# Performance work log

Measured on AMD Instinct MI355X. Metric: run time of the kernel, lower is better.

The kernel has to match this reference:

```python
import jax, jax.numpy as jnp
import numpy as np

EPS_ATTN = 1e-8  # self.eps is undefined in the torch source; standard slot-attention value
LN_EPS = 1e-5


def _ln(x, g=None, b=None, axes=(-1,)):
    m = x.mean(axes, keepdims=True)
    v = ((x - m) ** 2).mean(axes, keepdims=True)
    y = (x - m) * jax.lax.rsqrt(v + LN_EPS)
    return y * g + b if g is not None else y


def setup_inputs() -> dict:
    key = jax.random.key(0)
    ks = jax.random.split(key, 16)
    B, N, S, d, dh = 16, 4096, 8, 64, 128

    def w(k, shape, fan_in):
        return jax.random.normal(k, shape, jnp.float32) / np.float32(np.sqrt(fan_in))

    return {
        "inputs": jax.random.normal(ks[0], (B, N, d + 2), jnp.float32),
        "slots": jax.random.normal(ks[1], (S, d + 4), jnp.float32),
        "Wq": w(ks[2], (d, d), d),
        "Wk": w(ks[3], (d, d), d),
        "Wv": w(ks[4], (d, d), d),
        "Wg": w(ks[5], (d, 2), 2),
        "bg": jnp.zeros((d,), jnp.float32),
        "ln_pos_g": jnp.ones((d,), jnp.float32),
        "ln_pos_b": jnp.zeros((d,), jnp.float32),
        "W1": w(ks[6], (dh, d), d),
        "b1": jnp.zeros((dh,), jnp.float32),
        "W2": w(ks[7], (d, dh), dh),
        "b2": jnp.zeros((d,), jnp.float32),
        "W_ih": w(ks[8], (3 * d, d), d),
        "W_hh": w(ks[9], (3 * d, d), d),
        "b_ih": jnp.zeros((3 * d,), jnp.float32),
        "b_hh": jnp.zeros((3 * d,), jnp.float32),
        "ln_mlp_g": jnp.ones((d,), jnp.float32),
        "ln_mlp_b": jnp.zeros((d,), jnp.float32),
        "W3": w(ks[10], (dh, d), d),
        "b3": jnp.zeros((dh,), jnp.float32),
        "W4": w(ks[11], (d, dh), dh),
        "b4": jnp.zeros((d,), jnp.float32),
        "ln_slot_g": jnp.ones((d,), jnp.float32),
        "ln_slot_b": jnp.zeros((d,), jnp.float32),
        "n_iters": 3,
    }


def reference(inputs, slots, Wq, Wk, Wv, Wg, bg, ln_pos_g, ln_pos_b, W1, b1, W2, b2,
              W_ih, W_hh, b_ih, b_hh, ln_mlp_g, ln_mlp_b, W3, b3, W4, b4,
              ln_slot_g, ln_slot_b, n_iters):
    feats, grids = inputs[..., :-2], inputs[..., -2:]          # (B,N,d), (B,N,2)
    sl, pos, sc = slots[..., :-4], slots[..., -4:-2], slots[..., -2:]
    B, N, _ = feats.shape
    S, d = sl.shape
    scale = d ** (-0.5)

    slots = jnp.broadcast_to(sl, (B, S, d))
    positions = jnp.clip(jnp.broadcast_to(pos, (B, S, 2)), -1.0, 1.0)
    scales = jnp.clip(jnp.broadcast_to(sc, (B, S, 2)), 1e-3, 2.0)

    k = feats @ Wk.T                                           # (B,N,d)
    v = feats @ Wv.T

    def pos_mlp(x):  # LayerNorm -> Linear -> ReLU -> Linear
        h = _ln(x, ln_pos_g, ln_pos_b)
        h = jax.nn.relu(h @ W1.T + b1)
        return h @ W2.T + b2

    for i_iter in range(n_iters + 1):
        rel = (grids[:, :, None] - positions[:, None]) / scales[:, None]  # (B,N,S,2)
        rgp = rel @ Wg.T + bg                                             # (B,N,S,d)
        k_pos = pos_mlp(k[:, :, None] + rgp)                              # (B,N,S,d)
        v_pos = pos_mlp(v[:, :, None] + rgp)

        slots_n = _ln(slots, ln_slot_g, ln_slot_b)
        q = _ln(slots_n, axes=(-2, -1)) @ Wq.T                            # (B,S,d)

        dots = jnp.einsum('bsd,bnsd->bns', q, k_pos) * scale              # (B,N,S)
        attn = jax.nn.softmax(dots, axis=1) + EPS_ATTN
        attn = attn / attn.sum(axis=-1, keepdims=True)

        updates = jnp.einsum('bns,bnsd->bsd', attn, v_pos)                # (B,S,d)
        positions = jnp.einsum('bns,bnp->bsp', attn, grids)               # (B,S,2)
        spread = (grids[:, :, None] - positions[:, None]) ** 2            # (B,N,S,2)
        scales = jnp.clip(jnp.sqrt(jnp.einsum('bns,bnsp->bsp', attn, spread)), 1e-3, 2.0)

        if i_iter < n_iters:
            x = updates.reshape(-1, d)
            h = slots.reshape(-1, d)
            gi = x @ W_ih.T + b_ih
            gh = h @ W_hh.T + b_hh
            i_r, i_z, i_n = jnp.split(gi, 3, axis=-1)
            h_r, h_z, h_n = jnp.split(gh, 3, axis=-1)
            r = jax.nn.sigmoid(i_r + h_r)
            z = jax.nn.sigmoid(i_z + h_z)
            n_g = jnp.tanh(i_n + r * h_n)
            slots = ((1.0 - z) * n_g + z * h).reshape(B, S, d)
            # slot_mlp (no residual in the source)
            hmlp = jax.nn.relu(_ln(slots, ln_mlp_g, ln_mlp_b) @ W3.T + b3)
            slots = hmlp @ W4.T + b4

    return jnp.concatenate([slots, positions, scales], axis=-1)           # (B,S,d+4)
```

## Files before the change

### kernel.cpp

```cpp
#include <hip/hip_runtime.h>
#include <math.h>

#define BB 16
#define NN 4096
#define SS 8
#define DD 64
#define DHH 128
#define CIN 66
#define NITERS 3
#define LN_EPS_F 1e-5f
#define EPS_ATTN_F 1e-8f
#define QSCALE 0.125f
#define LO_SCALE 2048.0f
#define LO_INV 4.8828125e-4f

typedef __attribute__((ext_vector_type(8))) _Float16 half8;
typedef __attribute__((ext_vector_type(4))) float f32x4;
union H8 { half8 v; _Float16 u[8]; };

__device__ __forceinline__ float dot4(float4 a, float4 b) {
    return fmaf(a.x, b.x, fmaf(a.y, b.y, fmaf(a.z, b.z, a.w * b.w)));
}

__device__ __forceinline__ void split_fp16(float z, _Float16& h, _Float16& l) {
    _Float16 hh = (_Float16)z;
    float rem = (z - (float)hh) * LO_SCALE;
    h = hh;
    l = (_Float16)rem;
}

__global__ __launch_bounds__(256) void k_init_slots(
    const float* __restrict__ slots_in, float* __restrict__ slots,
    float* __restrict__ positions, float* __restrict__ scales) {
    int tid = blockIdx.x * 256 + threadIdx.x;
    if (tid < BB * SS * DD) {
        int s = (tid / DD) % SS;
        int c = tid % DD;
        slots[tid] = slots_in[s * 68 + c];
    }
    if (tid < BB * SS * 2) {
        int s = (tid >> 1) & 7;
        int p = tid & 1;
        float po = slots_in[s * 68 + 64 + p];
        positions[tid] = fminf(fmaxf(po, -1.f), 1.f);
        float sc = slots_in[s * 68 + 66 + p];
        scales[tid] = fminf(fmaxf(sc, 1e-3f), 2.f);
    }
}

__global__ __launch_bounds__(256) void k_prep_w(
    const float* __restrict__ W1, const float* __restrict__ lpg,
    const float* __restrict__ lpb, const float* __restrict__ b1,
    const float* __restrict__ Wg,
    float* __restrict__ W1p, float* __restrict__ avec, float* __restrict__ bvec,
    float* __restrict__ s1vec, float* __restrict__ b1p, float* __restrict__ wgc) {
    __shared__ float w1s[128 * 68];
    int tid = threadIdx.x;
    for (int q = 0; q < 8; q++) {
        int flat = q * 1024 + tid * 4;
        int o = flat >> 6, c = flat & 63;
        *(float4*)(w1s + o * 68 + c) = *(const float4*)(W1 + flat);
    }
    __syncthreads();
    if (tid < 128) {
        int o = tid;
        float a = 0.f, bv = 0.f, s1 = 0.f, b1a = b1[o];
        for (int c = 0; c < 64; c++) {
            float w0 = w1s[o * 68 + c];
            float w = w0 * lpg[c];
            W1p[o * 64 + c] = w;
            a = fmaf(w, Wg[2 * c], a);
            bv = fmaf(w, Wg[2 * c + 1], bv);
            s1 += w;
            b1a = fmaf(w0, lpb[c], b1a);
        }
        avec[o] = a; bvec[o] = bv; s1vec[o] = s1; b1p[o] = b1a;
    }
    if (tid == 128) {
        float mwA = 0.f, mwB = 0.f, AA = 0.f, BBv = 0.f, AB = 0.f;
        for (int c = 0; c < 64; c++) {
            float wa = Wg[2 * c], wb = Wg[2 * c + 1];
            mwA += wa; mwB += wb;
            AA = fmaf(wa, wa, AA); BBv = fmaf(wb, wb, BBv); AB = fmaf(wa, wb, AB);
        }
        wgc[0] = mwA * (1.f / 64.f);
        wgc[1] = mwB * (1.f / 64.f);
        wgc[2] = AA * (1.f / 64.f);
        wgc[3] = BBv * (1.f / 64.f);
        wgc[4] = AB * (2.f / 64.f);
    }
}

__global__ __launch_bounds__(256) void k_prep_w2(
    const float* __restrict__ W1p, const float* __restrict__ Wk,
    const float* __restrict__ Wv, const float* __restrict__ bg,
    float* __restrict__ Wall, float* __restrict__ cu) {
    int flat = blockIdx.x * 256 + threadIdx.x;
    int mat = flat >> 13, rem = flat & 8191;
    int o = rem >> 6, c = rem & 63;
    const float* Wm = mat ? Wv : Wk;
    float acc = 0.f;
    for (int d = 0; d < 64; d++)
        acc = fmaf(W1p[o * 64 + d], Wm[d * 64 + c], acc);
    Wall[flat] = acc;
    if (flat < 128) {
        float a = 0.f;
        for (int d = 0; d < 64; d++) a = fmaf(W1p[flat * 64 + d], bg[d], a);
        cu[flat] = a;
    }
}

__global__ __launch_bounds__(256) void k_prep_frag(
    const float* __restrict__ Wall, const float* __restrict__ Wk,
    const float* __restrict__ Wv,
    _Float16* __restrict__ cwh, _Float16* __restrict__ cwl,
    _Float16* __restrict__ mwh, _Float16* __restrict__ mwl) {
    int idx = blockIdx.x * 256 + threadIdx.x;
    if (idx < 2048) {
        int f = idx >> 6, lane = idx & 63;
        int m = f >> 4, rest = f & 15;
        int ot = rest >> 1, ks = rest & 1;
        int o = ot * 16 + (lane & 15);
        int k0 = ks * 32 + (lane >> 4) * 8;
        const float* src = Wall + m * 8192 + o * 64 + k0;
        #pragma unroll
        for (int j = 0; j < 8; j++) {
            _Float16 h, l;
            split_fp16(src[j], h, l);
            cwh[(size_t)f * 512 + lane * 8 + j] = h;
            cwl[(size_t)f * 512 + lane * 8 + j] = l;
        }
    } else if (idx < 3072) {
        int id2 = idx - 2048;
        int f = id2 >> 6, lane = id2 & 63;
        int m = f >> 3, rest = f & 7;
        int ot = rest >> 1, ks = rest & 1;
        int o = ot * 16 + (lane & 15);
        int k0 = ks * 32 + (lane >> 4) * 8;
        const float* src = (m ? Wv : Wk) + o * 64 + k0;
        #pragma unroll
        for (int j = 0; j < 8; j++) {
            _Float16 h, l;
            split_fp16(src[j], h, l);
            mwh[(size_t)f * 512 + lane * 8 + j] = h;
            mwl[(size_t)f * 512 + lane * 8 + j] = l;
        }
    }
}

__global__ __launch_bounds__(256) void k_prep_mfma(
    const float* __restrict__ inp,
    const _Float16* __restrict__ cwh, const _Float16* __restrict__ cwl,
    const _Float16* __restrict__ mwh, const _Float16* __restrict__ mwl,
    const float* __restrict__ cu, const float* __restrict__ bg,
    const float* __restrict__ Wg,
    float* __restrict__ uk, float* __restrict__ uv,
    float* __restrict__ kaux, float* __restrict__ vaux, float* __restrict__ gbuf) {
    int tid = threadIdx.x;
    int wv = tid >> 6, lane = tid & 63;
    int quad = lane >> 4, col = lane & 15;
    int mat = blockIdx.y;
    int rowTile = blockIdx.x * 64 + wv * 16;
    half8 ah[2], al[2];
    {
        int rA = rowTile + col;
        const float* rp = inp + (size_t)rA * CIN + quad * 8;
        #pragma unroll
        for (int ks = 0; ks < 2; ks++) {
            H8 h, l;
            #pragma unroll
            for (int q = 0; q < 4; q++) {
                float2 v = *(const float2*)(rp + ks * 32 + 2 * q);
                split_fp16(v.x, h.u[2 * q], l.u[2 * q]);
                split_fp16(v.y, h.u[2 * q + 1], l.u[2 * q + 1]);
            }
            ah[ks] = h.v; al[ks] = l.v;
        }
    }
    const _Float16* cwhm = cwh + (size_t)mat * 16 * 512;
    const _Float16* cwlm = cwl + (size_t)mat * 16 * 512;
    float* dst = mat ? uv : uk;
    float* outb = dst + (size_t)(rowTile + quad * 4) * 128 + col;
    #pragma unroll
    for (int ot = 0; ot < 8; ot++) {
        f32x4 acc1 = {0.f, 0.f, 0.f, 0.f}, acc2 = {0.f, 0.f, 0.f, 0.f};
        #pragma unroll
        for (int ks = 0; ks < 2; ks++) {
            half8 bh = *(const half8*)(cwhm + (size_t)(ot * 2 + ks) * 512 + lane * 8);
            half8 bl = *(const half8*)(cwlm + (size_t)(ot * 2 + ks) * 512 + lane * 8);
            acc1 = __builtin_amdgcn_mfma_f32_16x16x32_f16(ah[ks], bh, acc1, 0, 0, 0);
            acc2 = __builtin_amdgcn_mfma_f32_16x16x32_f16(al[ks], bh, acc2, 0, 0, 0);
            acc2 = __builtin_amdgcn_mfma_f32_16x16x32_f16(ah[ks], bl, acc2, 0, 0, 0);
        }
        float cuv = cu[ot * 16 + col];
        #pragma unroll
        for (int r = 0; r < 4; r++)
            outb[(size_t)r * 128 + ot * 16] = fmaf(acc2[r], LO_INV, acc1[r]) + cuv;
    }
    const _Float16* mwhm = mwh + (size_t)mat * 8 * 512;
    const _Float16* mwlm = mwl + (size_t)mat * 8 * 512;
    float mk[4] = {0.f, 0.f, 0.f, 0.f}, kk2[4] = {0.f, 0.f, 0.f, 0.f};
    float kA[4] = {0.f, 0.f, 0.f, 0.f}, kB[4] = {0.f, 0.f, 0.f, 0.f};
    #pragma unroll
    for (int ot = 0; ot < 4; ot++) {
        f32x4 acc1 = {0.f, 0.f, 0.f, 0.f}, acc2 = {0.f, 0.f, 0.f, 0.f};
        #pragma unroll
        for (int ks = 0; ks < 2; ks++) {
            half8 bh = *(const half8*)(mwhm + (size_t)(ot * 2 + ks) * 512 + lane * 8);
            half8 bl = *(const half8*)(mwlm + (size_t)(ot * 2 + ks) * 512 + lane * 8);
            acc1 = __builtin_amdgcn_mfma_f32_16x16x32_f16(ah[ks], bh, acc1, 0, 0, 0);
            acc2 = __builtin_amdgcn_mfma_f32_16x16x32_f16(al[ks], bh, acc2, 0, 0, 0);
            acc2 = __builtin_amdgcn_mfma_f32_16x16x32_f16(ah[ks], bl, acc2, 0, 0, 0);
        }
        int o = ot * 16 + col;
        float bgo = bg[o], wa = Wg[2 * o], wb = Wg[2 * o + 1];
        #pragma unroll
        for (int r = 0; r < 4; r++) {
            float x = fmaf(acc2[r], LO_INV, acc1[r]) + bgo;
            mk[r] += x; kk2[r] = fmaf(x, x, kk2[r]);
            kA[r] = fmaf(x, wa, kA[r]); kB[r] = fmaf(x, wb, kB[r]);
        }
    }
    #pragma unroll
    for (int off = 1; off <= 8; off <<= 1) {
        #pragma unroll
        for (int r = 0; r < 4; r++) {
            mk[r] += __shfl_xor(mk[r], off, 64);
            kk2[r] += __shfl_xor(kk2[r], off, 64);
            kA[r] += __shfl_xor(kA[r], off, 64);
            kB[r] += __shfl_xor(kB[r], off, 64);
        }
    }
    float* aux = mat ? vaux : kaux;
    if (col == 0) {
        #pragma unroll
        for (int r = 0; r < 4; r++) {
            int row = rowTile + quad * 4 + r;
            float2 g = *(const float2*)(inp + (size_t)row * CIN + 64);
            float4 m1 = {mk[r] * (1.f / 64.f), kk2[r] * (1.f / 64.f),
                         kA[r] * (1.f / 32.f), kB[r] * (1.f / 32.f)};
            float4 m2 = {g.x, g.y, 0.f, 0.f};
            *(float4*)(aux + (size_t)row * 8) = m1;
            *(float4*)(aux + (size_t)row * 8 + 4) = m2;
            if (mat == 0) {
                float2 gw = {g.x, g.y};
                *(float2*)(gbuf + (size_t)row * 2) = gw;
            }
        }
    }
}

__global__ __launch_bounds__(512) void k_slot_prep(
    const float* __restrict__ slots, const float* __restrict__ lsg,
    const float* __restrict__ lsb, const float* __restrict__ Wq,
    const float* __restrict__ W2, const float* __restrict__ b2,
    float* __restrict__ w2q, float* __restrict__ qb2) {
    __shared__ float sn[512];
    __shared__ float qv[SS][64];
    __shared__ float wsum[8], wsum2[8];
    int b = blockIdx.x, t = threadIdx.x;
    int s = t >> 6, c = t & 63;
    float x = slots[(b * SS + s) * DD + c];
    float sum = x;
    for (int off = 32; off; off >>= 1) sum += __shfl_xor(sum, off, 64);
    float m = sum * (1.f / 64.f);
    float dv = x - m;
    float vs = dv * dv;
    for (int off = 32; off; off >>= 1) vs += __shfl_xor(vs, off, 64);
    float y = dv * rsqrtf(vs * (1.f / 64.f) + LN_EPS_F) * lsg[c] + lsb[c];
    float s1 = y, s2 = y * y;
    for (int off = 32; off; off >>= 1) { s1 += __shfl_xor(s1, off, 64); s2 += __shfl_xor(s2, off, 64); }
    if (c == 0) { wsum[s] = s1; wsum2[s] = s2; }
    __syncthreads();
    float ts1 = 0.f, ts2 = 0.f;
    #pragma unroll
    for (int i = 0; i < 8; i++) { ts1 += wsum[i]; ts2 += wsum2[i]; }
    float gm = ts1 * (1.f / 512.f);
    float gv = ts2 * (1.f / 512.f) - gm * gm;
    sn[t] = (y - gm) * rsqrtf(gv + LN_EPS_F);
    __syncthreads();
    float acc = 0.f;
    for (int j4 = 0; j4 < 64; j4 += 4)
        acc += dot4(*(const float4*)&sn[s * 64 + j4], *(const float4*)(Wq + c * 64 + j4));
    qv[s][c] = acc;
    __syncthreads();
    float a0 = 0.f, a1 = 0.f;
    for (int cc = 0; cc < 64; cc++) {
        float qc = qv[s][cc];
        a0 = fmaf(qc, W2[cc * DHH + c], a0);
        a1 = fmaf(qc, W2[cc * DHH + c + 64], a1);
    }
    w2q[(b * SS + s) * DHH + c] = a0 * QSCALE;
    w2q[(b * SS + s) * DHH + c + 64] = a1 * QSCALE;
    float qb = qv[s][c] * b2[c];
    for (int off = 32; off; off >>= 1) qb += __shfl_xor(qb, off, 64);
    if (c == 0) qb2[b * SS + s] = qb * QSCALE;
}

__global__ __launch_bounds__(256) void k_pass1(
    const float* __restrict__ uk, const float* __restrict__ kaux,
    const float* __restrict__ positions, const float* __restrict__ scales,
    const float* __restrict__ avec, const float* __restrict__ bvec,
    const float* __restrict__ s1vec, const float* __restrict__ b1p,
    const float* __restrict__ wgc, const float* __restrict__ w2q,
    const float* __restrict__ qb2, float* __restrict__ dots) {
    int tid = threadIdx.x;
    int chunk = blockIdx.x, b = blockIdx.y;
    int wv = tid >> 6, lane = tid & 63, rh = lane >> 5, ol = lane & 31;
    int o4 = ol * 4;
    float4 a4 = *(const float4*)(avec + o4);
    float4 bv4 = *(const float4*)(bvec + o4);
    float4 s14 = *(const float4*)(s1vec + o4);
    float4 b14 = *(const float4*)(b1p + o4);
    float mwA = wgc[0], mwB = wgc[1], AA = wgc[2], BBc = wgc[3], AB2 = wgc[4];
    float p0[8], p1[8], rc0[8], rc1[8], qb[8];
    float4 wq[8];
    #pragma unroll
    for (int s = 0; s < 8; s++) {
        int bs = b * 8 + s;
        p0[s] = positions[bs * 2]; p1[s] = positions[bs * 2 + 1];
        rc0[s] = 1.f / scales[bs * 2]; rc1[s] = 1.f / scales[bs * 2 + 1];
        qb[s] = qb2[bs];
        wq[s] = *(const float4*)(w2q + (size_t)bs * DHH + o4);
    }
    int row0 = chunk * 64 + wv * 16 + rh;
    size_t rg = (size_t)b * NN + row0;
    float4 m1 = *(const float4*)(kaux + rg * 8);
    float4 m2 = *(const float4*)(kaux + rg * 8 + 4);
    float4 u4 = *(const float4*)(uk + rg * 128 + o4);
    for (int st = 0; st < 8; st++) {
        float4 n1, n2, nu;
        if (st < 7) {
            size_t rgn = rg + (size_t)(st + 1) * 2;
            n1 = *(const float4*)(kaux + rgn * 8);
            n2 = *(const float4*)(kaux + rgn * 8 + 4);
            nu = *(const float4*)(uk + rgn * 128 + o4);
        }
        int row = row0 + st * 2;
        #pragma unroll
        for (int s = 0; s < 8; s++) {
            float rel0 = (m2.x - p0[s]) * rc0[s];
            float rel1 = (m2.y - p1[s]) * rc1[s];
            float m = fmaf(rel1, mwB, fmaf(rel0, mwA, m1.x));
            float q2 = fmaf(rel0, fmaf(rel0, AA, m1.z), m1.y);
            q2 = fmaf(rel1, fmaf(rel1, BBc, m1.w), q2);
            q2 = fmaf(rel0 * rel1, AB2, q2);
            float var = fmaf(-m, m, q2);
            float rstd = rsqrtf(fmaxf(var, 0.f) + LN_EPS_F);
            float p = 0.f, t, h;
            t = fmaf(-m, s14.x, u4.x); t = fmaf(rel0, a4.x, t); t = fmaf(rel1, bv4.x, t);
            h = fmaf(rstd, t, b14.x); p = fmaf(fmaxf(h, 0.f), wq[s].x, p);
            t = fmaf(-m, s14.y, u4.y); t = fmaf(rel0, a4.y, t); t = fmaf(rel1, bv4.y, t);
            h = fmaf(rstd, t, b14.y); p = fmaf(fmaxf(h, 0.f), wq[s].y, p);
            t = fmaf(-m, s14.z, u4.z); t = fmaf(rel0, a4.z, t); t = fmaf(rel1, bv4.z, t);
            h = fmaf(rstd, t, b14.z); p = fmaf(fmaxf(h, 0.f), wq[s].z, p);
            t = fmaf(-m, s14.w, u4.w); t = fmaf(rel0, a4.w, t); t = fmaf(rel1, bv4.w, t);
            h = fmaf(rstd, t, b14.w); p = fmaf(fmaxf(h, 0.f), wq[s].w, p);
            p += __shfl_xor(p, 1, 64);
            p += __shfl_xor(p, 2, 64);
            p += __shfl_xor(p, 4, 64);
            p += __shfl_xor(p, 8, 64);
            p += __shfl_xor(p, 16, 64);
            if (ol == 0)
                dots[(size_t)(b * 8 + s) * NN + row] = p + qb[s];
        }
        m1 = n1; m2 = n2; u4 = nu;
    }
}

__global__ __launch_bounds__(256) void k_pass2(
    const float* __restrict__ uv, const float* __restrict__ vaux,
    const float* __restrict__ positions, const float* __restrict__ scales,
    const float* __restrict__ avec, const float* __restrict__ bvec,
    const float* __restrict__ s1vec, const float* __restrict__ b1p,
    const float* __restrict__ wgc, const float* __restrict__ attn,
    float* __restrict__ H) {
    __shared__ float Hw[4 * 1024];
    int tid = threadIdx.x;
    int chunk = blockIdx.x, b = blockIdx.y;
    int wv = tid >> 6, lane = tid & 63, rh = lane >> 5, ol = lane & 31;
    int o4 = ol * 4;
    float4 a4 = *(const float4*)(avec + o4);
    float4 bv4 = *(const float4*)(bvec + o4);
    float4 s14 = *(const float4*)(s1vec + o4);
    float4 b14 = *(const float4*)(b1p + o4);
    float mwA = wgc[0], mwB = wgc[1], AA = wgc[2], BBc = wgc[3], AB2 = wgc[4];
    float p0[8], p1[8], rc0[8], rc1[8];
    #pragma unroll
    for (int s = 0; s < 8; s++) {
        int bs = b * 8 + s;
        p0[s] = positions[bs * 2]; p1[s] = positions[bs * 2 + 1];
        rc0[s] = 1.f / scales[bs * 2]; rc1[s] = 1.f / scales[bs * 2 + 1];
    }
    float hq[8][4];
    #pragma unroll
    for (int s = 0; s < 8; s++)
        #pragma unroll
        for (int c = 0; c < 4; c++) hq[s][c] = 0.f;
    int row0 = chunk * 64 + wv * 16 + rh;
    size_t rg = (size_t)b * NN + row0;
    float4 m1 = *(const float4*)(vaux + rg * 8);
    float4 m2 = *(const float4*)(vaux + rg * 8 + 4);
    float4 u4 = *(const float4*)(uv + rg * 128 + o4);
    for (int st = 0; st < 8; st++) {
        float4 n1, n2, nu;
        if (st < 7) {
            size_t rgn = rg + (size_t)(st + 1) * 2;
            n1 = *(const float4*)(vaux + rgn * 8);
            n2 = *(const float4*)(vaux + rgn * 8 + 4);
            nu = *(const float4*)(uv + rgn * 128 + o4);
        }
        int row = row0 + st * 2;
        #pragma unroll
        for (int s = 0; s < 8; s++) {
            float ar = attn[(size_t)(b * 8 + s) * NN + row];
            float rel0 = (m2.x - p0[s]) * rc0[s];
            float rel1 = (m2.y - p1[s]) * rc1[s];
            float m = fmaf(rel1, mwB, fmaf(rel0, mwA, m1.x));
            float q2 = fmaf(rel0, fmaf(rel0, AA, m1.z), m1.y);
            q2 = fmaf(rel1, fmaf(rel1, BBc, m1.w), q2);
            q2 = fmaf(rel0 * rel1, AB2, q2);
            float var = fmaf(-m, m, q2);
            float rstd = rsqrtf(fmaxf(var, 0.f) + LN_EPS_F);
            float t, h;
            t = fmaf(-m, s14.x, u4.x); t = fmaf(rel0, a4.x, t); t = fmaf(rel1, bv4.x, t);
            h = fmaf(rstd, t, b14.x); hq[s][0] = fmaf(ar, fmaxf(h, 0.f), hq[s][0]);
            t = fmaf(-m, s14.y, u4.y); t = fmaf(rel0, a4.y, t); t = fmaf(rel1, bv4.y, t);
            h = fmaf(rstd, t, b14.y); hq[s][1] = fmaf(ar, fmaxf(h, 0.f), hq[s][1]);
            t = fmaf(-m, s14.z, u4.z); t = fmaf(rel0, a4.z, t); t = fmaf(rel1, bv4.z, t);
            h = fmaf(rstd, t, b14.z); hq[s][2] = fmaf(ar, fmaxf(h, 0.f), hq[s][2]);
            t = fmaf(-m, s14.w, u4.w); t = fmaf(rel0, a4.w, t); t = fmaf(rel1, bv4.w, t);
            h = fmaf(rstd, t, b14.w); hq[s][3] = fmaf(ar, fmaxf(h, 0.f), hq[s][3]);
        }
        m1 = n1; m2 = n2; u4 = nu;
    }
    #pragma unroll
    for (int s = 0; s < 8; s++)
        #pragma unroll
        for (int c = 0; c < 4; c++)
            hq[s][c] += __shfl_xor(hq[s][c], 32, 64);
    if (lane < 32) {
        #pragma unroll
        for (int s = 0; s < 8; s++) {
            float4 st = {hq[s][0], hq[s][1], hq[s][2], hq[s][3]};
            *(float4*)(Hw + wv * 1024 + s * 128 + o4) = st;
        }
    }
    __syncthreads();
    #pragma unroll
    for (int q = 0; q < 4; q++) {
        int flat = q * 256 + tid;
        float sum = Hw[flat] + Hw[1024 + flat] + Hw[2048 + flat] + Hw[3072 + flat];
        atomicAdd(&H[(size_t)b * 8 * DHH + flat], sum);
    }
}

__global__ __launch_bounds__(256) void k_softmax_ms(
    const float* __restrict__ dots, float* __restrict__ Mv, float* __restrict__ Lv,
    float* __restrict__ H, float* __restrict__ sacc) {
    __shared__ float red[4];
    int bs = blockIdx.x, t = threadIdx.x;
    if (t < 128) H[(size_t)bs * DHH + t] = 0.f;
    if (t < 8) sacc[bs * 8 + t] = 0.f;
    const float* dp = dots + (size_t)bs * NN;
    float mx = -1e30f;
    #pragma unroll
    for (int it = 0; it < 4; it++) {
        float4 d = *(const float4*)(dp + it * 1024 + t * 4);
        mx = fmaxf(mx, fmaxf(fmaxf(d.x, d.y), fmaxf(d.z, d.w)));
    }
    for (int off = 32; off; off >>= 1) mx = fmaxf(mx, __shfl_xor(mx, off, 64));
    if ((t & 63) == 0) red[t >> 6] = mx;
    __syncthreads();
    float M = fmaxf(fmaxf(red[0], red[1]), fmaxf(red[2], red[3]));
    __syncthreads();
    float sm = 0.f;
    #pragma unroll
    for (int it = 0; it < 4; it++) {
        float4 d = *(const float4*)(dp + it * 1024 + t * 4);
        sm += __expf(d.x - M) + __expf(d.y - M) + __expf(d.z - M) + __expf(d.w - M);
    }
    for (int off = 32; off; off >>= 1) sm += __shfl_xor(sm, off, 64);
    if ((t & 63) == 0) red[t >> 6] = sm;
    __syncthreads();
    if (t == 0) { Mv[bs] = M; Lv[bs] = red[0] + red[1] + red[2] + red[3]; }
}

__global__ __launch_bounds__(256) void k_attn_stats(
    const float* __restrict__ dots, const float* __restrict__ Mv,
    const float* __restrict__ Lv, const float* __restrict__ gbuf,
    float* __restrict__ attn, float* __restrict__ sacc) {
    __shared__ float red[4][40];
    int chunk = blockIdx.x, b = blockIdx.y;
    int t = threadIdx.x;
    int n = chunk * 256 + t;
    float2 g = *(const float2*)(gbuf + (size_t)(b * NN + n) * 2);
    float gx2 = g.x * g.x, gy2 = g.y * g.y;
    float a[8];
    float rs = 0.f;
    #pragma unroll
    for (int s = 0; s < 8; s++) {
        int bs = b * 8 + s;
        float d = dots[(size_t)bs * NN + n];
        a[s] = __expf(d - Mv[bs]) * (1.f / Lv[bs]) + EPS_ATTN_F;
        rs += a[s];
    }
    float inv = 1.f / rs;
    float v[8][5];
    #pragma unroll
    for (int s = 0; s < 8; s++) {
        float av = a[s] * inv;
        attn[(size_t)(b * 8 + s) * NN + n] = av;
        v[s][0] = av;
        v[s][1] = av * g.x;  v[s][2] = av * g.y;
        v[s][3] = av * gx2;  v[s][4] = av * gy2;
    }
    #pragma unroll
    for (int off = 1; off <= 32; off <<= 1)
        #pragma unroll
        for (int s = 0; s < 8; s++)
            #pragma unroll
            for (int j = 0; j < 5; j++)
                v[s][j] += __shfl_xor(v[s][j], off, 64);
    int lane = t & 63, wv = t >> 6;
    if (lane == 0) {
        #pragma unroll
        for (int s = 0; s < 8; s++)
            #pragma unroll
            for (int j = 0; j < 5; j++)
                red[wv][s * 5 + j] = v[s][j];
    }
    __syncthreads();
    if (t < 40) {
        float sum = red[0][t] + red[1][t] + red[2][t] + red[3][t];
        int s = t / 5, j = t % 5;
        atomicAdd(&sacc[(b * 8 + s) * 8 + j], sum);
    }
}

__global__ __launch_bounds__(64) void k_gru_mlp(
    const float* __restrict__ H, const float* __restrict__ sacc,
    const float* __restrict__ W2, const float* __restrict__ b2,
    const float* __restrict__ W_ih, const float* __restrict__ W_hh,
    const float* __restrict__ b_ih, const float* __restrict__ b_hh,
    const float* __restrict__ lmg, const float* __restrict__ lmb,
    const float* __restrict__ W3, const float* __restrict__ b3,
    const float* __restrict__ W4, const float* __restrict__ b4,
    float* __restrict__ slots, float* __restrict__ positions,
    float* __restrict__ scales) {
    int bs = blockIdx.x;
    int c = threadIdx.x;
    __shared__ float hl[DHH], ul[DD], sl[DD], yl[DD], hml[DHH];
    float A0 = sacc[bs * 8 + 0];
    if (c < 2) {
        float A1 = sacc[bs * 8 + 1 + c];
        float A2 = sacc[bs * 8 + 3 + c];
        positions[bs * 2 + c] = A1;
        float sx = A2 - A1 * A1 * (2.f - A0);
        scales[bs * 2 + c] = fminf(fmaxf(sqrtf(fmaxf(sx, 0.f)), 1e-3f), 2.f);
    }
    hl[c] = H[bs * DHH + c];
    hl[c + 64] = H[bs * DHH + 64 + c];
    float hold = slots[bs * DD + c];
    sl[c] = hold;
    __syncthreads();
    float u = A0 * b2[c];
    for (int o = 0; o < DHH; o += 4) {
        float4 w = *(const float4*)(W2 + c * DHH + o);
        u = fmaf(w.x, hl[o], fmaf(w.y, hl[o + 1], fmaf(w.z, hl[o + 2], fmaf(w.w, hl[o + 3], u))));
    }
    ul[c] = u;
    __syncthreads();
    float gir = b_ih[c], giz = b_ih[64 + c], gin = b_ih[128 + c];
    float ghr = b_hh[c], ghz = b_hh[64 + c], ghn = b_hh[128 + c];
    for (int k4 = 0; k4 < DD; k4 += 4) {
        float4 uu = *(const float4*)(ul + k4);
        float4 hh = *(const float4*)(sl + k4);
        gir += dot4(uu, *(const float4*)(W_ih + c * DD + k4));
        giz += dot4(uu, *(const float4*)(W_ih + (64 + c) * DD + k4));
        gin += dot4(uu, *(const float4*)(W_ih + (128 + c) * DD + k4));
        ghr += dot4(hh, *(const float4*)(W_hh + c * DD + k4));
        ghz += dot4(hh, *(const float4*)(W_hh + (64 + c) * DD + k4));
        ghn += dot4(hh, *(const float4*)(W_hh + (128 + c) * DD + k4));
    }
    float rg = 1.f / (1.f + expf(-(gir + ghr)));
    float zg = 1.f / (1.f + expf(-(giz + ghz)));
    float ng = tanhf(gin + rg * ghn);
    float snew = (1.f - zg) * ng + zg * hold;
    float sum = snew;
    for (int off = 32; off; off >>= 1) sum += __shfl_xor(sum, off, 64);
    float m = sum * (1.f / 64.f);
    float dv = snew - m;
    float vv = dv * dv;
    for (int off = 32; off; off >>= 1) vv += __shfl_xor(vv, off, 64);
    yl[c] = dv * rsqrtf(vv * (1.f / 64.f) + LN_EPS_F) * lmg[c] + lmb[c];
    __syncthreads();
    float h0 = b3[c], h1 = b3[64 + c];
    for (int k4 = 0; k4 < DD; k4 += 4) {
        float4 yy = *(const float4*)(yl + k4);
        h0 += dot4(yy, *(const float4*)(W3 + c * DD + k4));
        h1 += dot4(yy, *(const float4*)(W3 + (64 + c) * DD + k4));
    }
    hml[c] = fmaxf(h0, 0.f);
    hml[64 + c] = fmaxf(h1, 0.f);
    __syncthreads();
    float outv = b4[c];
    for (int o4 = 0; o4 < DHH; o4 += 4) {
        float4 hm4 = *(const float4*)(hml + o4);
        outv += dot4(hm4, *(const float4*)(W4 + c * DHH + o4));
    }
    slots[bs * DD + c] = outv;
}

__global__ __launch_bounds__(256) void k_write_out(
    const float* __restrict__ slots, const float* __restrict__ sacc,
    float* __restrict__ out) {
    int tid = blockIdx.x * 256 + threadIdx.x;
    if (tid >= BB * SS * 68) return;
    int bs = tid / 68, c = tid % 68;
    float v;
    if (c < 64) {
        v = slots[bs * 64 + c];
    } else if (c < 66) {
        v = sacc[bs * 8 + 1 + (c - 64)];
    } else {
        int p = c - 66;
        float A0 = sacc[bs * 8 + 0];
        float A1 = sacc[bs * 8 + 1 + p];
        float A2 = sacc[bs * 8 + 3 + p];
        float sx = A2 - A1 * A1 * (2.f - A0);
        v = fminf(fmaxf(sqrtf(fmaxf(sx, 0.f)), 1e-3f), 2.f);
    }
    out[tid] = v;
}

extern "C" void kernel_launch(void* const* d_in, const int* in_sizes, int n_in,
                              void* d_out, int out_size, void* d_ws, size_t ws_size,
                              hipStream_t stream) {
    (void)in_sizes; (void)n_in; (void)out_size; (void)ws_size;
    const float* inp = (const float*)d_in[0];
    const float* slots_in = (const float*)d_in[1];
    const float* Wq = (const float*)d_in[2];
    const float* Wk = (const float*)d_in[3];
    const float* Wv = (const float*)d_in[4];
    const float* Wg = (const float*)d_in[5];
    const float* bg = (const float*)d_in[6];
    const float* lpg = (const float*)d_in[7];
    const float* lpb = (const float*)d_in[8];
    const float* W1 = (const float*)d_in[9];
    const float* b1 = (const float*)d_in[10];
    const float* W2 = (const float*)d_in[11];
    const float* b2 = (const float*)d_in[12];
    const float* W_ih = (const float*)d_in[13];
    const float* W_hh = (const float*)d_in[14];
    const float* b_ih = (const float*)d_in[15];
    const float* b_hh = (const float*)d_in[16];
    const float* lmg = (const float*)d_in[17];
    const float* lmb = (const float*)d_in[18];
    const float* W3 = (const float*)d_in[19];
    const float* b3 = (const float*)d_in[20];
    const float* W4 = (const float*)d_in[21];
    const float* b4 = (const float*)d_in[22];
    const float* lsg = (const float*)d_in[23];
    const float* lsb = (const float*)d_in[24];
    float* out = (float*)d_out;
    float* ws = (float*)d_ws;

    const size_t NR = (size_t)BB * NN;
    size_t o_uk = 0;
    size_t o_uv = o_uk + NR * 128;
    size_t o_kaux = o_uv + NR * 128;
    size_t o_vaux = o_kaux + NR * 8;
    size_t o_gbuf = o_vaux + NR * 8;
    size_t o_dots = o_gbuf + NR * 2;
    size_t o_attn = o_dots + NR * SS;
    size_t o_slots = o_attn + NR * SS;
    size_t o_pos = o_slots + BB * SS * DD;
    size_t o_scl = o_pos + BB * SS * 2;
    size_t o_w2q = o_scl + BB * SS * 2;
    size_t o_qb2 = o_w2q + BB * SS * DHH;
    size_t o_Mv = o_qb2 + BB * SS;
    size_t o_Lv = o_Mv + BB * SS;
    size_t o_H = o_Lv + BB * SS;
    size_t o_sacc = o_H + BB * SS * DHH;
    size_t o_W1p = o_sacc + BB * SS * 8;
    size_t o_avec = o_W1p + DHH * DD;
    size_t o_bvec = o_avec + DHH;
    size_t o_s1v = o_bvec + DHH;
    size_t o_b1p = o_s1v + DHH;
    size_t o_wgc = o_b1p + DHH;
    size_t o_Wall = o_wgc + 8;
    size_t o_cu = o_Wall + 2 * DHH * DD;
    size_t o_cwh = o_cu + DHH;
    size_t o_cwl = o_cwh + 8192;
    size_t o_mwh = o_cwl + 8192;
    size_t o_mwl = o_mwh + 4096;

    float* uk = ws + o_uk;
    float* uv = ws + o_uv;
    float* kaux = ws + o_kaux;
    float* vaux = ws + o_vaux;
    float* gbuf = ws + o_gbuf;
    float* dots = ws + o_dots;
    float* attn = ws + o_attn;
    float* slots = ws + o_slots;
    float* positions = ws + o_pos;
    float* scales = ws + o_scl;
    float* w2q = ws + o_w2q;
    float* qb2 = ws + o_qb2;
    float* Mv = ws + o_Mv;
    float* Lv = ws + o_Lv;
    float* H = ws + o_H;
    float* sacc = ws + o_sacc;
    float* W1p = ws + o_W1p;
    float* avec = ws + o_avec;
    float* bvec = ws + o_bvec;
    float* s1v = ws + o_s1v;
    float* b1p = ws + o_b1p;
    float* wgc = ws + o_wgc;
    float* Wall = ws + o_Wall;
    float* cu = ws + o_cu;
    _Float16* cwh = (_Float16*)(ws + o_cwh);
    _Float16* cwl = (_Float16*)(ws + o_cwl);
    _Float16* mwh = (_Float16*)(ws + o_mwh);
    _Float16* mwl = (_Float16*)(ws + o_mwl);

    k_init_slots<<<32, 256, 0, stream>>>(slots_in, slots, positions, scales);
    k_prep_w<<<1, 256, 0, stream>>>(W1, lpg, lpb, b1, Wg, W1p, avec, bvec, s1v, b1p, wgc);
    k_prep_w2<<<64, 256, 0, stream>>>(W1p, Wk, Wv, bg, Wall, cu);
    k_prep_frag<<<12, 256, 0, stream>>>(Wall, Wk, Wv, cwh, cwl, mwh, mwl);
    k_prep_mfma<<<dim3(1024, 2), 256, 0, stream>>>(inp, cwh, cwl, mwh, mwl,
                                                   cu, bg, Wg, uk, uv, kaux, vaux, gbuf);

    for (int it = 0; it <= NITERS; ++it) {
        k_slot_prep<<<BB, 512, 0, stream>>>(slots, lsg, lsb, Wq, W2, b2, w2q, qb2);
        k_pass1<<<dim3(64, BB), 256, 0, stream>>>(uk, kaux, positions, scales,
                                                  avec, bvec, s1v, b1p, wgc, w2q, qb2, dots);
        k_softmax_ms<<<BB * SS, 256, 0, stream>>>(dots, Mv, Lv, H, sacc);
        k_attn_stats<<<dim3(16, BB), 256, 0, stream>>>(dots, Mv, Lv, gbuf, attn, sacc);
        if (it < NITERS) {
            k_pass2<<<dim3(64, BB), 256, 0, stream>>>(uv, vaux, positions, scales,
                                                      avec, bvec, s1v, b1p, wgc, attn, H);
            k_gru_mlp<<<BB * SS, 64, 0, stream>>>(H, sacc, W2, b2, W_ih, W_hh, b_ih, b_hh,
                                                  lmg, lmb, W3, b3, W4, b4,
                                                  slots, positions, scales);
        }
    }
    k_write_out<<<34, 256, 0, stream>>>(slots, sacc, out);
}
```

Baseline: 443.3 us.

## Fuse softmax max/sum and attention stats into one per-batch kernel

Merges the separate softmax max/sum kernel and the attention statistics kernel into one 1024-thread block per batch, which computes the max, the normaliser, the normalized attention and the position/scale moments in a single launch. The per-slot sums are now written directly instead of accumulated with atomics. Writing attn is skipped on the final iteration, where nothing reads it. Smaller tweaks split k_slot_prep across two blocks per batch and use fast __expf in the GRU sigmoids. In exchange, only 16 blocks launch for the fused kernel, so parallelism drops, and the dots buffer is read three times inside each block.

New measurement: 482.7 us. 1.09x slower.

```diff
diff --git a/kernel.cpp b/kernel.cpp
--- a/kernel.cpp
+++ b/kernel.cpp
@@ -258,7 +258,7 @@
     __shared__ float sn[512];
     __shared__ float qv[SS][64];
     __shared__ float wsum[8], wsum2[8];
-    int b = blockIdx.x, t = threadIdx.x;
+    int b = blockIdx.x, half = blockIdx.y, t = threadIdx.x;
     int s = t >> 6, c = t & 63;
     float x = slots[(b * SS + s) * DD + c];
     float sum = x;
@@ -284,17 +284,15 @@
         acc += dot4(*(const float4*)&sn[s * 64 + j4], *(const float4*)(Wq + c * 64 + j4));
     qv[s][c] = acc;
     __syncthreads();
-    float a0 = 0.f, a1 = 0.f;
-    for (int cc = 0; cc < 64; cc++) {
-        float qc = qv[s][cc];
-        a0 = fmaf(qc, W2[cc * DHH + c], a0);
-        a1 = fmaf(qc, W2[cc * DHH + c + 64], a1);
-    }
-    w2q[(b * SS + s) * DHH + c] = a0 * QSCALE;
-    w2q[(b * SS + s) * DHH + c + 64] = a1 * QSCALE;
-    float qb = qv[s][c] * b2[c];
-    for (int off = 32; off; off >>= 1) qb += __shfl_xor(qb, off, 64);
-    if (c == 0) qb2[b * SS + s] = qb * QSCALE;
+    float a0 = 0.f;
+    for (int cc = 0; cc < 64; cc++)
+        a0 = fmaf(qv[s][cc], W2[cc * DHH + c + half * 64], a0);
+    w2q[(b * SS + s) * DHH + c + half * 64] = a0 * QSCALE;
+    if (half == 0) {
+        float qb = qv[s][c] * b2[c];
+        for (int off = 32; off; off >>= 1) qb += __shfl_xor(qb, off, 64);
+        if (c == 0) qb2[b * SS + s] = qb * QSCALE;
+    }
 }
 
 __global__ __launch_bounds__(256) void k_pass1(
@@ -455,86 +453,124 @@
     }
 }
 
-__global__ __launch_bounds__(256) void k_softmax_ms(
-    const float* __restrict__ dots, float* __restrict__ Mv, float* __restrict__ Lv,
-    float* __restrict__ H, float* __restrict__ sacc) {
-    __shared__ float red[4];
-    int bs = blockIdx.x, t = threadIdx.x;
-    if (t < 128) H[(size_t)bs * DHH + t] = 0.f;
-    if (t < 8) sacc[bs * 8 + t] = 0.f;
-    const float* dp = dots + (size_t)bs * NN;
-    float mx = -1e30f;
-    #pragma unroll
-    for (int it = 0; it < 4; it++) {
-        float4 d = *(const float4*)(dp + it * 1024 + t * 4);
-        mx = fmaxf(mx, fmaxf(fmaxf(d.x, d.y), fmaxf(d.z, d.w)));
-    }
-    for (int off = 32; off; off >>= 1) mx = fmaxf(mx, __shfl_xor(mx, off, 64));
-    if ((t & 63) == 0) red[t >> 6] = mx;
-    __syncthreads();
-    float M = fmaxf(fmaxf(red[0], red[1]), fmaxf(red[2], red[3]));
-    __syncthreads();
-    float sm = 0.f;
-    #pragma unroll
-    for (int it = 0; it < 4; it++) {
-        float4 d = *(const float4*)(dp + it * 1024 + t * 4);
-        sm += __expf(d.x - M) + __expf(d.y - M) + __expf(d.z - M) + __expf(d.w - M);
-    }
-    for (int off = 32; off; off >>= 1) sm += __shfl_xor(sm, off, 64);
-    if ((t & 63) == 0) red[t >> 6] = sm;
-    __syncthreads();
-    if (t == 0) { Mv[bs] = M; Lv[bs] = red[0] + red[1] + red[2] + red[3]; }
-}
-
-__global__ __launch_bounds__(256) void k_attn_stats(
-    const float* __restrict__ dots, const float* __restrict__ Mv,
-    const float* __restrict__ Lv, const float* __restrict__ gbuf,
-    float* __restrict__ attn, float* __restrict__ sacc) {
-    __shared__ float red[4][40];
-    int chunk = blockIdx.x, b = blockIdx.y;
+template<bool WRITE_ATTN>
+__global__ __launch_bounds__(1024) void k_softmax_stats(
+    const float* __restrict__ dots, const float* __restrict__ gbuf,
+    float* __restrict__ attn, float* __restrict__ H, float* __restrict__ sacc) {
+    __shared__ float redw[16][8];
+    __shared__ float bM[8], bLi[8];
+    __shared__ float sred[16][40];
+    int b = blockIdx.x;
     int t = threadIdx.x;
-    int n = chunk * 256 + t;
-    float2 g = *(const float2*)(gbuf + (size_t)(b * NN + n) * 2);
-    float gx2 = g.x * g.x, gy2 = g.y * g.y;
-    float a[8];
-    float rs = 0.f;
-    #pragma unroll
-    for (int s = 0; s < 8; s++) {
-        int bs = b * 8 + s;
-        float d = dots[(size_t)bs * NN + n];
-        a[s] = __expf(d - Mv[bs]) * (1.f / Lv[bs]) + EPS_ATTN_F;
-        rs += a[s];
-    }
-    float inv = 1.f / rs;
-    float v[8][5];
-    #pragma unroll
-    for (int s = 0; s < 8; s++) {
-        float av = a[s] * inv;
-        attn[(size_t)(b * 8 + s) * NN + n] = av;
-        v[s][0] = av;
-        v[s][1] = av * g.x;  v[s][2] = av * g.y;
-        v[s][3] = av * gx2;  v[s][4] = av * gy2;
-    }
-    #pragma unroll
-    for (int off = 1; off <= 32; off <<= 1)
-        #pragma unroll
-        for (int s = 0; s < 8; s++)
+    int wv = t >> 6, lane = t & 63;
+    int n0 = t * 4;
+    H[(size_t)b * 8 * DHH + t] = 0.f;
+    {
+        float m8[8];
+        #pragma unroll
+        for (int s = 0; s < 8; s++) {
+            float4 d = *(const float4*)(dots + (size_t)(b * 8 + s) * NN + n0);
+            m8[s] = fmaxf(fmaxf(d.x, d.y), fmaxf(d.z, d.w));
+        }
+        #pragma unroll
+        for (int off = 32; off; off >>= 1)
             #pragma unroll
-            for (int j = 0; j < 5; j++)
-                v[s][j] += __shfl_xor(v[s][j], off, 64);
-    int lane = t & 63, wv = t >> 6;
+            for (int s = 0; s < 8; s++)
+                m8[s] = fmaxf(m8[s], __shfl_xor(m8[s], off, 64));
+        if (lane == 0) {
+            #pragma unroll
+            for (int s = 0; s < 8; s++) redw[wv][s] = m8[s];
+        }
+    }
+    __syncthreads();
+    if (t < 8) {
+        float M = redw[0][t];
+        #pragma unroll
+        for (int w = 1; w < 16; w++) M = fmaxf(M, redw[w][t]);
+        bM[t] = M;
+    }
+    __syncthreads();
+    {
+        float l8[8];
+        #pragma unroll
+        for (int s = 0; s < 8; s++) {
+            float4 d = *(const float4*)(dots + (size_t)(b * 8 + s) * NN + n0);
+            float M = bM[s];
+            l8[s] = __expf(d.x - M) + __expf(d.y - M) + __expf(d.z - M) + __expf(d.w - M);
+        }
+        #pragma unroll
+        for (int off = 32; off; off >>= 1)
+            #pragma unroll
+            for (int s = 0; s < 8; s++)
+                l8[s] += __shfl_xor(l8[s], off, 64);
+        if (lane == 0) {
+            #pragma unroll
+            for (int s = 0; s < 8; s++) redw[wv][s] = l8[s];
+        }
+    }
+    __syncthreads();
+    if (t < 8) {
+        float L = 0.f;
+        #pragma unroll
+        for (int w = 0; w < 16; w++) L += redw[w][t];
+        bLi[t] = 1.f / L;
+    }
+    __syncthreads();
+    float v0[8], v1[8], v2[8], v3[8], v4[8];
+    #pragma unroll
+    for (int s = 0; s < 8; s++) { v0[s] = 0.f; v1[s] = 0.f; v2[s] = 0.f; v3[s] = 0.f; v4[s] = 0.f; }
+    #pragma unroll
+    for (int j = 0; j < 4; j++) {
+        int n = n0 + j;
+        float2 g = *(const float2*)(gbuf + (size_t)(b * NN + n) * 2);
+        float e[8], rs = 0.f;
+        #pragma unroll
+        for (int s = 0; s < 8; s++) {
+            float d = dots[(size_t)(b * 8 + s) * NN + n];
+            e[s] = __expf(d - bM[s]) * bLi[s] + EPS_ATTN_F;
+            rs += e[s];
+        }
+        float inv = 1.f / rs;
+        float gx2 = g.x * g.x, gy2 = g.y * g.y;
+        #pragma unroll
+        for (int s = 0; s < 8; s++) {
+            float av = e[s] * inv;
+            if (WRITE_ATTN)
+                attn[(size_t)(b * 8 + s) * NN + n] = av;
+            v0[s] += av;
+            v1[s] = fmaf(av, g.x, v1[s]);
+            v2[s] = fmaf(av, g.y, v2[s]);
+            v3[s] = fmaf(av, gx2, v3[s]);
+            v4[s] = fmaf(av, gy2, v4[s]);
+        }
+    }
+    #pragma unroll
+    for (int off = 32; off; off >>= 1)
+        #pragma unroll
+        for (int s = 0; s < 8; s++) {
+            v0[s] += __shfl_xor(v0[s], off, 64);
+            v1[s] += __shfl_xor(v1[s], off, 64);
+            v2[s] += __shfl_xor(v2[s], off, 64);
+            v3[s] += __shfl_xor(v3[s], off, 64);
+            v4[s] += __shfl_xor(v4[s], off, 64);
+        }
     if (lane == 0) {
         #pragma unroll
-        for (int s = 0; s < 8; s++)
-            #pragma unroll
-            for (int j = 0; j < 5; j++)
-                red[wv][s * 5 + j] = v[s][j];
+        for (int s = 0; s < 8; s++) {
+            sred[wv][s * 5 + 0] = v0[s];
+            sred[wv][s * 5 + 1] = v1[s];
+            sred[wv][s * 5 + 2] = v2[s];
+            sred[wv][s * 5 + 3] = v3[s];
+            sred[wv][s * 5 + 4] = v4[s];
+        }
     }
     __syncthreads();
     if (t < 40) {
-        float sum = red[0][t] + red[1][t] + red[2][t] + red[3][t];
+        float sum = 0.f;
+        #pragma unroll
+        for (int w = 0; w < 16; w++) sum += sred[w][t];
         int s = t / 5, j = t % 5;
-        atomicAdd(&sacc[(b * 8 + s) * 8 + j], sum);
+        sacc[(b * 8 + s) * 8 + j] = sum;
     }
 }
 
@@ -583,8 +619,8 @@
         ghz += dot4(hh, *(const float4*)(W_hh + (64 + c) * DD + k4));
         ghn += dot4(hh, *(const float4*)(W_hh + (128 + c) * DD + k4));
     }
-    float rg = 1.f / (1.f + expf(-(gir + ghr)));
-    float zg = 1.f / (1.f + expf(-(giz + ghz)));
+    float rg = 1.f / (1.f + __expf(-(gir + ghr)));
+    float zg = 1.f / (1.f + __expf(-(giz + ghz)));
     float ng = tanhf(gin + rg * ghn);
     float snew = (1.f - zg) * ng + zg * hold;
     float sum = snew;
@@ -679,9 +715,7 @@
     size_t o_scl = o_pos + BB * SS * 2;
     size_t o_w2q = o_scl + BB * SS * 2;
     size_t o_qb2 = o_w2q + BB * SS * DHH;
-    size_t o_Mv = o_qb2 + BB * SS;
-    size_t o_Lv = o_Mv + BB * SS;
-    size_t o_H = o_Lv + BB * SS;
+    size_t o_H = o_qb2 + BB * SS;
     size_t o_sacc = o_H + BB * SS * DHH;
     size_t o_W1p = o_sacc + BB * SS * 8;
     size_t o_avec = o_W1p + DHH * DD;
@@ -708,8 +742,6 @@
     float* scales = ws + o_scl;
     float* w2q = ws + o_w2q;
     float* qb2 = ws + o_qb2;
-    float* Mv = ws + o_Mv;
-    float* Lv = ws + o_Lv;
     float* H = ws + o_H;
     float* sacc = ws + o_sacc;
     float* W1p = ws + o_W1p;
@@ -733,17 +765,18 @@
                                                    cu, bg, Wg, uk, uv, kaux, vaux, gbuf);
 
     for (int it = 0; it <= NITERS; ++it) {
-        k_slot_prep<<<BB, 512, 0, stream>>>(slots, lsg, lsb, Wq, W2, b2, w2q, qb2);
+        k_slot_prep<<<dim3(BB, 2), 512, 0, stream>>>(slots, lsg, lsb, Wq, W2, b2, w2q, qb2);
         k_pass1<<<dim3(64, BB), 256, 0, stream>>>(uk, kaux, positions, scales,
                                                   avec, bvec, s1v, b1p, wgc, w2q, qb2, dots);
-        k_softmax_ms<<<BB * SS, 256, 0, stream>>>(dots, Mv, Lv, H, sacc);
-        k_attn_stats<<<dim3(16, BB), 256, 0, stream>>>(dots, Mv, Lv, gbuf, attn, sacc);
         if (it < NITERS) {
+            k_softmax_stats<true><<<BB, 1024, 0, stream>>>(dots, gbuf, attn, H, sacc);
             k_pass2<<<dim3(64, BB), 256, 0, stream>>>(uv, vaux, positions, scales,
                                                       avec, bvec, s1v, b1p, wgc, attn, H);
             k_gru_mlp<<<BB * SS, 64, 0, stream>>>(H, sacc, W2, b2, W_ih, W_hh, b_ih, b_hh,
                                                   lmg, lmb, W3, b3, W4, b4,
                                                   slots, positions, scales);
+        } else {
+            k_softmax_stats<false><<<BB, 1024, 0, stream>>>(dots, gbuf, attn, H, sacc);
         }
     }
     k_write_out<<<34, 256, 0, stream>>>(slots, sacc, out);
```

## Fuse softmax max into pass1 with transposed shuffle reduction and atomics

Applied to the files above, without the earlier changes.

Pass1 now reduces the eight per-slot dot products with a butterfly transpose-reduction, so each shuffle stage handles several slots at once instead of running five shuffles per slot. Each lane also tracks a running max and publishes it with an order-preserving uint atomicMax. This lets the softmax kernel skip its separate max pass over dots. The final iteration no longer writes attn, and the GRU sigmoids use fast __expf. This adds atomics and a reset in slot_prep, and __expf carries slight accuracy risk.

After: 459.6 us. 1.04x slower.

```diff
diff --git a/kernel.cpp b/kernel.cpp
--- a/kernel.cpp
+++ b/kernel.cpp
@@ -27,6 +27,14 @@
     float rem = (z - (float)hh) * LO_SCALE;
     h = hh;
     l = (_Float16)rem;
+}
+
+__device__ __forceinline__ unsigned fmap(float f) {
+    unsigned u = __float_as_uint(f);
+    return (u & 0x80000000u) ? ~u : (u | 0x80000000u);
+}
+__device__ __forceinline__ float funmap(unsigned u) {
+    return __uint_as_float((u & 0x80000000u) ? (u ^ 0x80000000u) : ~u);
 }
 
 __global__ __launch_bounds__(256) void k_init_slots(
@@ -254,12 +262,14 @@
     const float* __restrict__ slots, const float* __restrict__ lsg,
     const float* __restrict__ lsb, const float* __restrict__ Wq,
     const float* __restrict__ W2, const float* __restrict__ b2,
-    float* __restrict__ w2q, float* __restrict__ qb2) {
+    float* __restrict__ w2q, float* __restrict__ qb2,
+    unsigned* __restrict__ Mbuf) {
     __shared__ float sn[512];
     __shared__ float qv[SS][64];
     __shared__ float wsum[8], wsum2[8];
     int b = blockIdx.x, t = threadIdx.x;
     int s = t >> 6, c = t & 63;
+    if (t < 8) Mbuf[b * 8 + t] = 0u;
     float x = slots[(b * SS + s) * DD + c];
     float sum = x;
     for (int off = 32; off; off >>= 1) sum += __shfl_xor(sum, off, 64);
@@ -303,7 +313,8 @@
     const float* __restrict__ avec, const float* __restrict__ bvec,
     const float* __restrict__ s1vec, const float* __restrict__ b1p,
     const float* __restrict__ wgc, const float* __restrict__ w2q,
-    const float* __restrict__ qb2, float* __restrict__ dots) {
+    const float* __restrict__ qb2, float* __restrict__ dots,
+    unsigned* __restrict__ Mbuf) {
     int tid = threadIdx.x;
     int chunk = blockIdx.x, b = blockIdx.y;
     int wv = tid >> 6, lane = tid & 63, rh = lane >> 5, ol = lane & 31;
@@ -323,6 +334,9 @@
         qb[s] = qb2[bs];
         wq[s] = *(const float4*)(w2q + (size_t)bs * DHH + o4);
     }
+    int sb4 = (ol >> 4) & 1, sb3 = (ol >> 3) & 1, sb2 = (ol >> 2) & 1;
+    int sofl = sb4 | (sb3 << 1) | (sb2 << 2);
+    float runM = -1e30f;
     int row0 = chunk * 64 + wv * 16 + rh;
     size_t rg = (size_t)b * NN + row0;
     float4 m1 = *(const float4*)(kaux + rg * 8);
@@ -337,6 +351,7 @@
             nu = *(const float4*)(uk + rgn * 128 + o4);
         }
         int row = row0 + st * 2;
+        float ps[8];
         #pragma unroll
         for (int s = 0; s < 8; s++) {
             float rel0 = (m2.x - p0[s]) * rc0[s];
@@ -356,16 +371,40 @@
             h = fmaf(rstd, t, b14.z); p = fmaf(fmaxf(h, 0.f), wq[s].z, p);
             t = fmaf(-m, s14.w, u4.w); t = fmaf(rel0, a4.w, t); t = fmaf(rel1, bv4.w, t);
             h = fmaf(rstd, t, b14.w); p = fmaf(fmaxf(h, 0.f), wq[s].w, p);
-            p += __shfl_xor(p, 1, 64);
-            p += __shfl_xor(p, 2, 64);
-            p += __shfl_xor(p, 4, 64);
-            p += __shfl_xor(p, 8, 64);
-            p += __shfl_xor(p, 16, 64);
-            if (ol == 0)
-                dots[(size_t)(b * 8 + s) * NN + row] = p + qb[s];
+            if (ol == 0) p += qb[s];
+            ps[s] = p;
+        }
+        float r4[4];
+        #pragma unroll
+        for (int j = 0; j < 4; j++) {
+            float ta = __shfl_xor(ps[2 * j], 16, 64);
+            float tb = __shfl_xor(ps[2 * j + 1], 16, 64);
+            r4[j] = sb4 ? (ps[2 * j + 1] + tb) : (ps[2 * j] + ta);
+        }
+        float r2[2];
+        #pragma unroll
+        for (int i = 0; i < 2; i++) {
+            float ta = __shfl_xor(r4[2 * i], 8, 64);
+            float tb = __shfl_xor(r4[2 * i + 1], 8, 64);
+            r2[i] = sb3 ? (r4[2 * i + 1] + tb) : (r4[2 * i] + ta);
+        }
+        {
+            float ta = __shfl_xor(r2[0], 4, 64);
+            float tb = __shfl_xor(r2[1], 4, 64);
+            float r = sb2 ? (r2[1] + tb) : (r2[0] + ta);
+            r += __shfl_xor(r, 2, 64);
+            r += __shfl_xor(r, 1, 64);
+            runM = fmaxf(runM, r);
+            if ((ol & 3) == 0)
+                dots[(size_t)(b * 8 + sofl) * NN + row] = r;
         }
         m1 = n1; m2 = n2; u4 = nu;
     }
+    runM = fmaxf(runM, __shfl_xor(runM, 1, 64));
+    runM = fmaxf(runM, __shfl_xor(runM, 2, 64));
+    runM = fmaxf(runM, __shfl_xor(runM, 32, 64));
+    if (lane < 32 && (ol & 3) == 0)
+        atomicMax(&Mbuf[b * 8 + sofl], fmap(runM));
 }
 
 __global__ __launch_bounds__(256) void k_pass2(
@@ -456,24 +495,15 @@
 }
 
 __global__ __launch_bounds__(256) void k_softmax_ms(
-    const float* __restrict__ dots, float* __restrict__ Mv, float* __restrict__ Lv,
+    const float* __restrict__ dots, const unsigned* __restrict__ Mbuf,
+    float* __restrict__ Mv, float* __restrict__ Lv,
     float* __restrict__ H, float* __restrict__ sacc) {
     __shared__ float red[4];
     int bs = blockIdx.x, t = threadIdx.x;
     if (t < 128) H[(size_t)bs * DHH + t] = 0.f;
     if (t < 8) sacc[bs * 8 + t] = 0.f;
+    float M = funmap(Mbuf[bs]);
     const float* dp = dots + (size_t)bs * NN;
-    float mx = -1e30f;
-    #pragma unroll
-    for (int it = 0; it < 4; it++) {
-        float4 d = *(const float4*)(dp + it * 1024 + t * 4);
-        mx = fmaxf(mx, fmaxf(fmaxf(d.x, d.y), fmaxf(d.z, d.w)));
-    }
-    for (int off = 32; off; off >>= 1) mx = fmaxf(mx, __shfl_xor(mx, off, 64));
-    if ((t & 63) == 0) red[t >> 6] = mx;
-    __syncthreads();
-    float M = fmaxf(fmaxf(red[0], red[1]), fmaxf(red[2], red[3]));
-    __syncthreads();
     float sm = 0.f;
     #pragma unroll
     for (int it = 0; it < 4; it++) {
@@ -486,6 +516,7 @@
     if (t == 0) { Mv[bs] = M; Lv[bs] = red[0] + red[1] + red[2] + red[3]; }
 }
 
+template<bool WRITE_ATTN>
 __global__ __launch_bounds__(256) void k_attn_stats(
     const float* __restrict__ dots, const float* __restrict__ Mv,
     const float* __restrict__ Lv, const float* __restrict__ gbuf,
@@ -510,7 +541,8 @@
     #pragma unroll
     for (int s = 0; s < 8; s++) {
         float av = a[s] * inv;
-        attn[(size_t)(b * 8 + s) * NN + n] = av;
+        if (WRITE_ATTN)
+            attn[(size_t)(b * 8 + s) * NN + n] = av;
         v[s][0] = av;
         v[s][1] = av * g.x;  v[s][2] = av * g.y;
         v[s][3] = av * gx2;  v[s][4] = av * gy2;
@@ -583,8 +615,8 @@
         ghz += dot4(hh, *(const float4*)(W_hh + (64 + c) * DD + k4));
         ghn += dot4(hh, *(const float4*)(W_hh + (128 + c) * DD + k4));
     }
-    float rg = 1.f / (1.f + expf(-(gir + ghr)));
-    float zg = 1.f / (1.f + expf(-(giz + ghz)));
+    float rg = 1.f / (1.f + __expf(-(gir + ghr)));
+    float zg = 1.f / (1.f + __expf(-(giz + ghz)));
     float ng = tanhf(gin + rg * ghn);
     float snew = (1.f - zg) * ng + zg * hold;
     float sum = snew;
@@ -681,7 +713,8 @@
     size_t o_qb2 = o_w2q + BB * SS * DHH;
     size_t o_Mv = o_qb2 + BB * SS;
     size_t o_Lv = o_Mv + BB * SS;
-    size_t o_H = o_Lv + BB * SS;
+    size_t o_Mb = o_Lv + BB * SS;
+    size_t o_H = o_Mb + BB * SS;
     size_t o_sacc = o_H + BB * SS * DHH;
     size_t o_W1p = o_sacc + BB * SS * 8;
     size_t o_avec = o_W1p + DHH * DD;
@@ -710,6 +743,7 @@
     float* qb2 = ws + o_qb2;
     float* Mv = ws + o_Mv;
     float* Lv = ws + o_Lv;
+    unsigned* Mbuf = (unsigned*)(ws + o_Mb);
     float* H = ws + o_H;
     float* sacc = ws + o_sacc;
     float* W1p = ws + o_W1p;
@@ -733,17 +767,20 @@
                                                    cu, bg, Wg, uk, uv, kaux, vaux, gbuf);
 
     for (int it = 0; it <= NITERS; ++it) {
-        k_slot_prep<<<BB, 512, 0, stream>>>(slots, lsg, lsb, Wq, W2, b2, w2q, qb2);
+        k_slot_prep<<<BB, 512, 0, stream>>>(slots, lsg, lsb, Wq, W2, b2, w2q, qb2, Mbuf);
         k_pass1<<<dim3(64, BB), 256, 0, stream>>>(uk, kaux, positions, scales,
-                                                  avec, bvec, s1v, b1p, wgc, w2q, qb2, dots);
-        k_softmax_ms<<<BB * SS, 256, 0, stream>>>(dots, Mv, Lv, H, sacc);
-        k_attn_stats<<<dim3(16, BB), 256, 0, stream>>>(dots, Mv, Lv, gbuf, attn, sacc);
+                                                  avec, bvec, s1v, b1p, wgc, w2q, qb2,
+                                                  dots, Mbuf);
+        k_softmax_ms<<<BB * SS, 256, 0, stream>>>(dots, Mbuf, Mv, Lv, H, sacc);
         if (it < NITERS) {
+            k_attn_stats<true><<<dim3(16, BB), 256, 0, stream>>>(dots, Mv, Lv, gbuf, attn, sacc);
             k_pass2<<<dim3(64, BB), 256, 0, stream>>>(uv, vaux, positions, scales,
                                                       avec, bvec, s1v, b1p, wgc, attn, H);
             k_gru_mlp<<<BB * SS, 64, 0, stream>>>(H, sacc, W2, b2, W_ih, W_hh, b_ih, b_hh,
                                                   lmg, lmb, W3, b3, W4, b4,
                                                   slots, positions, scales);
+        } else {
+            k_attn_stats<false><<<dim3(16, BB), 256, 0, stream>>>(dots, Mv, Lv, gbuf, attn, sacc);
         }
     }
     k_write_out<<<34, 256, 0, stream>>>(slots, sacc, out);
```
